# Kernel optimization log

Hardware: AMD Instinct MI355X
Metric: run time of the kernel (lower is better)

## Reference

```python
import jax, jax.numpy as jnp
import numpy as np

D_MODEL = 1024
NUM_HEADS = 16


def setup_inputs() -> dict:
    key = jax.random.key(0)
    ks = jax.random.split(key, 5)
    B, S, D = 2, 2048, D_MODEL
    x = jax.random.normal(ks[0], (B, S, D), dtype=jnp.float32)
    # nn.Linear(d_model, d_model, bias=False) weights, shape [out, in]
    scale = 1.0 / np.sqrt(D)
    Wq = jax.random.normal(ks[1], (D, D), dtype=jnp.float32) * scale
    Wk = jax.random.normal(ks[2], (D, D), dtype=jnp.float32) * scale
    Wv = jax.random.normal(ks[3], (D, D), dtype=jnp.float32) * scale
    Wo = jax.random.normal(ks[4], (D, D), dtype=jnp.float32) * scale
    return {"x": x, "Wq": Wq, "Wk": Wk, "Wv": Wv, "Wo": Wo}


def reference(x, Wq, Wk, Wv, Wo):
    B, S, D = x.shape
    H = NUM_HEADS
    dh = D // H
    # projections: x @ W.T (Linear without bias)
    q = (x @ Wq.T).reshape(B, S, H, dh).transpose(0, 2, 1, 3)  # [B,H,S,dh]
    k = (x @ Wk.T).reshape(B, S, H, dh).transpose(0, 2, 1, 3)
    v = (x @ Wv.T).reshape(B, S, H, dh).transpose(0, 2, 1, 3)
    scores = jnp.einsum("bhqd,bhkd->bhqk", q, k) / jnp.sqrt(jnp.float32(dh))
    # causal mask: positions j > i get -inf before softmax
    causal = jnp.triu(jnp.ones((S, S), dtype=bool), k=1)
    scores = jnp.where(causal, -jnp.inf, scores)
    attn = jax.nn.softmax(scores, axis=-1)  # [B,H,S,S]
    out = jnp.einsum("bhqk,bhkd->bhqd", attn, v)  # [B,H,S,dh]
    out = out.transpose(0, 2, 1, 3).reshape(B, S, D)
    return out @ Wo.T
```

## Files before the change

kernel.cpp:

```cpp
#include <hip/hip_runtime.h>

typedef __attribute__((ext_vector_type(8))) __bf16 bf16x8;
typedef __attribute__((ext_vector_type(4))) __bf16 bf16x4;
typedef __attribute__((ext_vector_type(2))) __bf16 bf16x2;
typedef __attribute__((ext_vector_type(4))) float f32x4;
typedef __attribute__((ext_vector_type(16))) float f32x16;
typedef __attribute__((ext_vector_type(4))) unsigned uint4v;

static constexpr int S = 2048;
static constexpr int D = 1024;
static constexpr int BATCH = 2;
static constexpr int M_ROWS = BATCH * S;

#define GLOAD_LDS16(gp, lp)                                                        \
  __builtin_amdgcn_global_load_lds((const __attribute__((address_space(1))) void*)(gp), \
                                   (__attribute__((address_space(3))) void*)(lp), 16, 0, 0)

__global__ __launch_bounds__(256) void cast_f32_bf16(const float* __restrict__ in,
                                                     __bf16* __restrict__ out) {
  int i = (blockIdx.x * 256 + threadIdx.x) * 4;
  *reinterpret_cast<bf16x4*>(out + i) =
      __builtin_convertvector(*reinterpret_cast<const f32x4*>(in + i), bf16x4);
}

__global__ __launch_bounds__(256) void cast_w4(const float* __restrict__ w0, const float* __restrict__ w1,
                                               const float* __restrict__ w2, const float* __restrict__ w3,
                                               __bf16* __restrict__ o0, __bf16* __restrict__ o1,
                                               __bf16* __restrict__ o2, __bf16* __restrict__ o3) {
  const float* in = blockIdx.y == 0 ? w0 : blockIdx.y == 1 ? w1 : blockIdx.y == 2 ? w2 : w3;
  __bf16* out = blockIdx.y == 0 ? o0 : blockIdx.y == 1 ? o1 : blockIdx.y == 2 ? o2 : o3;
  int i = (blockIdx.x * 256 + threadIdx.x) * 4;
  *reinterpret_cast<bf16x4*>(out + i) =
      __builtin_convertvector(*reinterpret_cast<const f32x4*>(in + i), bf16x4);
}

template <typename OutT>
__device__ __forceinline__ void gemm_core(const __bf16* __restrict__ A,
                                          const __bf16* __restrict__ Bm,
                                          OutT* __restrict__ C, int m0, int n0, int K, int ldc,
                                          __bf16* At, __bf16* Bt) {
  const int tid = threadIdx.x;
  const int w = tid >> 6, l = tid & 63;
  const int wr = w >> 1, wc = w & 1;
  const int ln = l & 15, gr = l >> 4;

  const int srow = w * 32 + (l >> 2);
  const int scol = (l & 3) * 8;
  const size_t aoff = (size_t)(m0 + srow) * K + scol;
  const size_t boff = (size_t)(n0 + srow) * K + scol;
  __bf16* lA = At + w * 2 * 512;
  __bf16* lB = Bt + w * 2 * 512;

  f32x4 acc[4][4] = {};

  for (int k0 = 0; k0 < K; k0 += 32) {
    __syncthreads();
    GLOAD_LDS16(A + aoff + k0, lA);
    GLOAD_LDS16(A + aoff + (size_t)16 * K + k0, lA + 512);
    GLOAD_LDS16(Bm + boff + k0, lB);
    GLOAD_LDS16(Bm + boff + (size_t)16 * K + k0, lB + 512);
    __syncthreads();

    bf16x8 af[4], bfr[4];
#pragma unroll
    for (int mi = 0; mi < 4; mi++)
      af[mi] = *reinterpret_cast<const bf16x8*>(&At[(wr * 64 + mi * 16 + ln) * 32 + gr * 8]);
#pragma unroll
    for (int ni = 0; ni < 4; ni++)
      bfr[ni] = *reinterpret_cast<const bf16x8*>(&Bt[(wc * 64 + ni * 16 + ln) * 32 + gr * 8]);
#pragma unroll
    for (int mi = 0; mi < 4; mi++)
#pragma unroll
      for (int ni = 0; ni < 4; ni++)
        acc[mi][ni] = __builtin_amdgcn_mfma_f32_16x16x32_bf16(af[mi], bfr[ni], acc[mi][ni], 0, 0, 0);
  }

#pragma unroll
  for (int mi = 0; mi < 4; mi++)
#pragma unroll
    for (int ni = 0; ni < 4; ni++)
#pragma unroll
      for (int r = 0; r < 4; r++) {
        int row = m0 + wr * 64 + mi * 16 + gr * 4 + r;
        int col = n0 + wc * 64 + ni * 16 + ln;
        float v = acc[mi][ni][r];
        if constexpr (__is_same(OutT, float))
          C[(size_t)row * ldc + col] = v;
        else
          C[(size_t)row * ldc + col] = (__bf16)v;
      }
}

__global__ __launch_bounds__(256) void qkv_gemm(const __bf16* __restrict__ xb,
                                                const __bf16* __restrict__ wq,
                                                const __bf16* __restrict__ wk,
                                                const __bf16* __restrict__ wv,
                                                __bf16* __restrict__ q, __bf16* __restrict__ k,
                                                __bf16* __restrict__ vt) {
  __shared__ __bf16 At[128 * 32];
  __shared__ __bf16 Bt[128 * 32];
  const int id = blockIdx.x;
  const __bf16 *A, *B;
  __bf16* C;
  int m0, n0, ldc;
  if (id < 512) {
    A = xb;
    B = (id < 256) ? wq : wk;
    C = (id < 256) ? q : k;
    int t = id & 255;
    m0 = (t >> 3) * 128;
    n0 = (t & 7) * 128;
    ldc = 1024;
  } else {
    int t = id - 512;
    A = wv;
    B = xb;
    C = vt;
    m0 = (t & 7) * 128;
    n0 = (t >> 3) * 128;
    ldc = 4096;
  }
  gemm_core<__bf16>(A, B, C, m0, n0, 1024, ldc, At, Bt);
}

__global__ __launch_bounds__(256) void wo_gemm(const __bf16* __restrict__ ob,
                                               const __bf16* __restrict__ wo,
                                               float* __restrict__ out) {
  __shared__ __bf16 At[128 * 32];
  __shared__ __bf16 Bt[128 * 32];
  gemm_core<float>(ob, wo, out, blockIdx.y * 128, blockIdx.x * 128, 1024, 1024, At, Bt);
}

__global__ __launch_bounds__(512, 2) void attn_kernel(const __bf16* __restrict__ Qb,
                                                      const __bf16* __restrict__ Kb,
                                                      const __bf16* __restrict__ VTb,
                                                      __bf16* __restrict__ Ob) {
  __shared__ __bf16 mo[8][64][32];
  __shared__ float mml[8][64][2];

  const int lin = blockIdx.x;
  const int wid = ((lin & 7) << 5) | (lin >> 3);
  const int bh = wid >> 3;
  const int ib = wid & 7;
  const int b = bh >> 4, h = bh & 15;

  const int tid = threadIdx.x;
  const int w = tid >> 6, l = tid & 63;
  const int q31 = l & 31, hi = l >> 5;
  const int pp = w & 3, hf = w >> 2;

  const int j = ib * 4 + pp;
  const int q0A = j * 32, q0B = (63 - j) * 32;
  const int nA = j + 1, nB = 64 - j;
  const int nhA = (nA + 1) >> 1, nhB = (nB + 1) >> 1;
  const int sA = hf ? nhA : 0, cA = hf ? nA - nhA : nhA;
  const int sB = hf ? nhB : 0, cB = hf ? nB - nhB : nhB;

  const __bf16* Qp = Qb + (size_t)b * S * D + h * 64;
  const __bf16* Kp = Kb + (size_t)b * S * D + h * 64;
  const __bf16* Vt = VTb + (size_t)(h * 64) * M_ROWS + b * S;

  const float SCALE2 = 0.125f * 1.44269504f;
  const float NEG = -1e30f;
  const float THR_RAW = 8.0f / SCALE2;

  bf16x8 qfA[4], qfB[4];
#pragma unroll
  for (int ds = 0; ds < 4; ds++) {
    qfA[ds] = *reinterpret_cast<const bf16x8*>(Qp + (size_t)(q0A + q31) * D + ds * 16 + hi * 8);
    qfB[ds] = *reinterpret_cast<const bf16x8*>(Qp + (size_t)(q0B + q31) * D + ds * 16 + hi * 8);
  }

  f32x16 oaccA[2] = {}, oaccB[2] = {};
  float mrA = NEG, lsA = 0.f, mrB = NEG, lsB = 0.f;

  auto loadK = [&](bf16x8 (&dst)[4], int kk) {
#pragma unroll
    for (int ds = 0; ds < 4; ds++)
      dst[ds] = *reinterpret_cast<const bf16x8*>(
          Kp + (size_t)(kk + q31) * D + ds * 16 + hi * 8);
  };
  auto loadV = [&](bf16x8 (&dst)[2][2], int kk) {
#pragma unroll
    for (int d0 = 0; d0 < 2; d0++)
#pragma unroll
      for (int ks = 0; ks < 2; ks++)
        dst[d0][ks] = *reinterpret_cast<const bf16x8*>(
            Vt + (size_t)(d0 * 32 + q31) * M_ROWS + kk + ks * 16 + hi * 8);
  };
  auto qk1 = [&](f32x16& st, bf16x8 (&kf)[4], bf16x8 (&qf)[4]) {
    f32x16 z = {};
#pragma unroll
    for (int ds = 0; ds < 4; ds++)
      z = __builtin_amdgcn_mfma_f32_32x32x16_bf16(kf[ds], qf[ds], z, 0, 0, 0);
    st = z;
  };
  auto pack2 = [](float x, float y) -> unsigned {
    bf16x2 p;
    p[0] = (__bf16)x;
    p[1] = (__bf16)y;
    return __builtin_bit_cast(unsigned, p);
  };
  auto maskmax = [&](f32x16& st, bool tail, float (&pv)[16]) -> float {
#pragma unroll
    for (int r = 0; r < 16; r++) {
      float v = st[r];
      if (tail) {
        int keyidx = (r & 3) + 8 * (r >> 2) + 4 * hi;
        v = (keyidx <= q31) ? v : NEG;
      }
      pv[r] = v;
    }
    float t8[8], t4[4];
#pragma unroll
    for (int ii = 0; ii < 8; ii++) t8[ii] = fmaxf(pv[ii], pv[ii + 8]);
#pragma unroll
    for (int ii = 0; ii < 4; ii++) t4[ii] = fmaxf(t8[ii], t8[ii + 4]);
    float tm = fmaxf(fmaxf(t4[0], t4[1]), fmaxf(t4[2], t4[3]));
    return fmaxf(tm, __shfl_xor(tm, 32));
  };
  auto rescale = [&](float& mr, float& ls, f32x16& o0, f32x16& o1, float tm) {
    float nm = fmaxf(mr, tm);
    float a = __builtin_exp2f((mr - nm) * SCALE2);
    mr = nm;
    ls *= a;
#pragma unroll
    for (int r = 0; r < 16; r++) o0[r] *= a;
#pragma unroll
    for (int r = 0; r < 16; r++) o1[r] *= a;
  };
  auto expsum = [&](float (&pv)[16], float mr, float& ls, unsigned (&dw)[8]) {
    const float mrs = mr * SCALE2;
#pragma unroll
    for (int r = 0; r < 16; r++)
      pv[r] = __builtin_exp2f(__builtin_fmaf(pv[r], SCALE2, -mrs));
    float s8[8], s4[4];
#pragma unroll
    for (int ii = 0; ii < 8; ii++) s8[ii] = pv[ii] + pv[ii + 8];
#pragma unroll
    for (int ii = 0; ii < 4; ii++) s4[ii] = s8[ii] + s8[ii + 4];
    float ps = (s4[0] + s4[1]) + (s4[2] + s4[3]);
    ps += __shfl_xor(ps, 32);
    ls += ps;
#pragma unroll
    for (int bb = 0; bb < 4; bb++) {
      dw[2 * bb] = pack2(pv[4 * bb], pv[4 * bb + 1]);
      dw[2 * bb + 1] = pack2(pv[4 * bb + 2], pv[4 * bb + 3]);
    }
  };
  auto pvmma = [&](unsigned (&dw)[8], bf16x8 (&vf)[2][2], f32x16& o0, f32x16& o1) {
#pragma unroll
    for (int ks = 0; ks < 2; ks++) {
      unsigned s0v = hi ? dw[4 * ks + 0] : dw[4 * ks + 2];
      unsigned s1v = hi ? dw[4 * ks + 1] : dw[4 * ks + 3];
      unsigned r0 = (unsigned)__shfl_xor((int)s0v, 32);
      unsigned r1 = (unsigned)__shfl_xor((int)s1v, 32);
      uint4v uv;
      uv.x = hi ? r0 : dw[4 * ks + 0];
      uv.y = hi ? r1 : dw[4 * ks + 1];
      uv.z = hi ? dw[4 * ks + 2] : r0;
      uv.w = hi ? dw[4 * ks + 3] : r1;
      bf16x8 pb = __builtin_bit_cast(bf16x8, uv);
      o0 = __builtin_amdgcn_mfma_f32_32x32x16_bf16(vf[0][ks], pb, o0, 0, 0, 0);
      o1 = __builtin_amdgcn_mfma_f32_32x32x16_bf16(vf[1][ks], pb, o1, 0, 0, 0);
    }
  };

  bf16x8 kfA[4], kfB[4], vfA[2][2], vfB[2][2];
  f32x16 stA, stB;

  if (cA > 0) {
    loadK(kfA, sA * 32);
    loadV(vfA, sA * 32);
  }
  loadK(kfB, sB * 32);
  loadV(vfB, sB * 32);

  for (int i2 = 0; i2 < cA; i2++) {
    __builtin_amdgcn_s_setprio(1);
    qk1(stA, kfA, qfA);
    qk1(stB, kfB, qfB);
    __builtin_amdgcn_s_setprio(0);
    if (i2 + 1 < cA) loadK(kfA, (sA + i2 + 1) * 32);
    if (i2 + 1 < cB) loadK(kfB, (sB + i2 + 1) * 32);

    float pvA[16], pvB[16];
    float tmA = maskmax(stA, sA + i2 == nA - 1, pvA);
    float tmB = maskmax(stB, sB + i2 == nB - 1, pvB);
    if (!__all((tmA - mrA <= THR_RAW) && (tmB - mrB <= THR_RAW))) {
      rescale(mrA, lsA, oaccA[0], oaccA[1], tmA);
      rescale(mrB, lsB, oaccB[0], oaccB[1], tmB);
    }
    unsigned dwA[8], dwB[8];
    expsum(pvA, mrA, lsA, dwA);
    expsum(pvB, mrB, lsB, dwB);
    __builtin_amdgcn_s_setprio(1);
    pvmma(dwA, vfA, oaccA[0], oaccA[1]);
    pvmma(dwB, vfB, oaccB[0], oaccB[1]);
    __builtin_amdgcn_s_setprio(0);
    if (i2 + 1 < cA) loadV(vfA, (sA + i2 + 1) * 32);
    if (i2 + 1 < cB) loadV(vfB, (sB + i2 + 1) * 32);
  }
  for (int i2 = cA; i2 < cB; i2++) {
    __builtin_amdgcn_s_setprio(1);
    qk1(stB, kfB, qfB);
    __builtin_amdgcn_s_setprio(0);
    if (i2 + 1 < cB) loadK(kfB, (sB + i2 + 1) * 32);
    float pvB[16];
    float tmB = maskmax(stB, sB + i2 == nB - 1, pvB);
    if (!__all(tmB - mrB <= THR_RAW)) rescale(mrB, lsB, oaccB[0], oaccB[1], tmB);
    unsigned dwB[8];
    expsum(pvB, mrB, lsB, dwB);
    __builtin_amdgcn_s_setprio(1);
    pvmma(dwB, vfB, oaccB[0], oaccB[1]);
    __builtin_amdgcn_s_setprio(0);
    if (i2 + 1 < cB) loadV(vfB, (sB + i2 + 1) * 32);
  }

  if (hf == 1) {
#pragma unroll
    for (int d0 = 0; d0 < 2; d0++) {
      bf16x8 pkA, pkB;
#pragma unroll
      for (int rr = 0; rr < 8; rr++) {
        pkA[rr] = (__bf16)oaccA[d0][rr];
        pkB[rr] = (__bf16)oaccB[d0][rr];
      }
      *reinterpret_cast<bf16x8*>(&mo[2 * pp + 0][l][d0 * 16]) = pkA;
      *reinterpret_cast<bf16x8*>(&mo[2 * pp + 1][l][d0 * 16]) = pkB;
      bf16x8 pkA2, pkB2;
#pragma unroll
      for (int rr = 0; rr < 8; rr++) {
        pkA2[rr] = (__bf16)oaccA[d0][8 + rr];
        pkB2[rr] = (__bf16)oaccB[d0][8 + rr];
      }
      *reinterpret_cast<bf16x8*>(&mo[2 * pp + 0][l][d0 * 16 + 8]) = pkA2;
      *reinterpret_cast<bf16x8*>(&mo[2 * pp + 1][l][d0 * 16 + 8]) = pkB2;
    }
    mml[2 * pp + 0][l][0] = mrA;
    mml[2 * pp + 0][l][1] = lsA;
    mml[2 * pp + 1][l][0] = mrB;
    mml[2 * pp + 1][l][1] = lsB;
  }
  __syncthreads();
  if (hf == 0) {
#pragma unroll
    for (int cc = 0; cc < 2; cc++) {
      const int slot = 2 * pp + cc;
      const int q0 = cc ? q0B : q0A;
      f32x16* oacc = cc ? oaccB : oaccA;
      float mr = cc ? mrB : mrA;
      float ls = cc ? lsB : lsA;
      float mr1 = mml[slot][l][0], ls1 = mml[slot][l][1];
      float mc = fmaxf(mr, mr1);
      float a0 = __builtin_exp2f((mr - mc) * SCALE2);
      float a1 = __builtin_exp2f((mr1 - mc) * SCALE2);
      float inv = 1.0f / (ls * a0 + ls1 * a1);
      float f0 = a0 * inv, f1 = a1 * inv;
      size_t row = (size_t)(b * S + q0 + q31);
#pragma unroll
      for (int d0 = 0; d0 < 2; d0++)
#pragma unroll
        for (int bb = 0; bb < 4; bb++) {
          bf16x4 ov;
#pragma unroll
          for (int rr = 0; rr < 4; rr++) {
            float part = (float)mo[slot][l][d0 * 16 + 4 * bb + rr];
            ov[rr] = (__bf16)(oacc[d0][4 * bb + rr] * f0 + part * f1);
          }
          *reinterpret_cast<bf16x4*>(Ob + row * D + h * 64 + d0 * 32 + 8 * bb + 4 * hi) = ov;
        }
    }
  }
}

extern "C" void kernel_launch(void* const* d_in, const int* in_sizes, int n_in,
                              void* d_out, int out_size, void* d_ws, size_t ws_size,
                              hipStream_t stream) {
  const float* x = (const float*)d_in[0];
  const float* Wq = (const float*)d_in[1];
  const float* Wk = (const float*)d_in[2];
  const float* Wv = (const float*)d_in[3];
  const float* Wo = (const float*)d_in[4];
  float* out = (float*)d_out;

  char* ws = (char*)d_ws;
  const size_t MB = 1024 * 1024;
  __bf16* xb = (__bf16*)(ws + 0 * MB);
  __bf16* qb = (__bf16*)(ws + 8 * MB);
  __bf16* kb = (__bf16*)(ws + 16 * MB);
  __bf16* vtb = (__bf16*)(ws + 24 * MB);
  __bf16* ob = (__bf16*)(ws + 32 * MB);
  __bf16* wqb = (__bf16*)(ws + 40 * MB);
  __bf16* wkb = (__bf16*)(ws + 42 * MB);
  __bf16* wvb = (__bf16*)(ws + 44 * MB);
  __bf16* wob = (__bf16*)(ws + 46 * MB);

  const int nx = M_ROWS * D;
  const int nw = D * D;

  cast_f32_bf16<<<nx / 4 / 256, 256, 0, stream>>>(x, xb);
  cast_w4<<<dim3(nw / 4 / 256, 4), 256, 0, stream>>>(Wq, Wk, Wv, Wo, wqb, wkb, wvb, wob);

  qkv_gemm<<<768, 256, 0, stream>>>(xb, wqb, wkb, wvb, qb, kb, vtb);

  attn_kernel<<<256, 512, 0, stream>>>(qb, kb, vtb, ob);

  wo_gemm<<<dim3(8, 32), 256, 0, stream>>>(ob, wob, out);
}
```

Baseline: 141.7 us.

## Split attention KV range across four wave groups with 4-way merge

The attention kernel now launches 1024-thread blocks and splits each query tile's causal KV range into four contiguous quarters instead of two halves. Each of the three non-leader wave groups writes its partial output, running max and sum to enlarged shared memory, and the leader merges four partial softmax states. The goal is more waves per block to hide latency and shorten the per-wave serial KV loop. In exchange it uses more LDS, drops the two-blocks-per-CU launch bound (which can raise register pressure or lower occupancy), and adds merge work.

```diff
diff --git a/kernel.cpp b/kernel.cpp
--- a/kernel.cpp
+++ b/kernel.cpp
@@ -131,12 +131,12 @@
   gemm_core<float>(ob, wo, out, blockIdx.y * 128, blockIdx.x * 128, 1024, 1024, At, Bt);
 }
 
-__global__ __launch_bounds__(512, 2) void attn_kernel(const __bf16* __restrict__ Qb,
-                                                      const __bf16* __restrict__ Kb,
-                                                      const __bf16* __restrict__ VTb,
-                                                      __bf16* __restrict__ Ob) {
-  __shared__ __bf16 mo[8][64][32];
-  __shared__ float mml[8][64][2];
+__global__ __launch_bounds__(1024) void attn_kernel(const __bf16* __restrict__ Qb,
+                                                    const __bf16* __restrict__ Kb,
+                                                    const __bf16* __restrict__ VTb,
+                                                    __bf16* __restrict__ Ob) {
+  __shared__ __bf16 mo[24][64][32];
+  __shared__ float mml[24][64][2];
 
   const int lin = blockIdx.x;
   const int wid = ((lin & 7) << 5) | (lin >> 3);
@@ -147,14 +147,13 @@
   const int tid = threadIdx.x;
   const int w = tid >> 6, l = tid & 63;
   const int q31 = l & 31, hi = l >> 5;
-  const int pp = w & 3, hf = w >> 2;
+  const int pp = w & 3, qq = w >> 2;
 
   const int j = ib * 4 + pp;
   const int q0A = j * 32, q0B = (63 - j) * 32;
   const int nA = j + 1, nB = 64 - j;
-  const int nhA = (nA + 1) >> 1, nhB = (nB + 1) >> 1;
-  const int sA = hf ? nhA : 0, cA = hf ? nA - nhA : nhA;
-  const int sB = hf ? nhB : 0, cB = hf ? nB - nhB : nhB;
+  const int sA = (nA * qq) >> 2, cA = ((nA * (qq + 1)) >> 2) - sA;
+  const int sB = (nB * qq) >> 2, cB = ((nB * (qq + 1)) >> 2) - sB;
 
   const __bf16* Qp = Qb + (size_t)b * S * D + h * 64;
   const __bf16* Kp = Kb + (size_t)b * S * D + h * 64;
@@ -273,8 +272,10 @@
     loadK(kfA, sA * 32);
     loadV(vfA, sA * 32);
   }
-  loadK(kfB, sB * 32);
-  loadV(vfB, sB * 32);
+  if (cB > 0) {
+    loadK(kfB, sB * 32);
+    loadV(vfB, sB * 32);
+  }
 
   for (int i2 = 0; i2 < cA; i2++) {
     __builtin_amdgcn_s_setprio(1);
@@ -317,46 +318,48 @@
     if (i2 + 1 < cB) loadV(vfB, (sB + i2 + 1) * 32);
   }
 
-  if (hf == 1) {
-#pragma unroll
-    for (int d0 = 0; d0 < 2; d0++) {
-      bf16x8 pkA, pkB;
-#pragma unroll
-      for (int rr = 0; rr < 8; rr++) {
-        pkA[rr] = (__bf16)oaccA[d0][rr];
-        pkB[rr] = (__bf16)oaccB[d0][rr];
+  if (qq != 0) {
+    const int base = (qq - 1) * 8 + pp * 2;
+#pragma unroll
+    for (int cc = 0; cc < 2; cc++) {
+      const f32x16* oacc = cc ? oaccB : oaccA;
+      const int slot = base + cc;
+#pragma unroll
+      for (int d0 = 0; d0 < 2; d0++) {
+        bf16x8 pk0, pk1;
+#pragma unroll
+        for (int rr = 0; rr < 8; rr++) {
+          pk0[rr] = (__bf16)oacc[d0][rr];
+          pk1[rr] = (__bf16)oacc[d0][8 + rr];
+        }
+        *reinterpret_cast<bf16x8*>(&mo[slot][l][d0 * 16]) = pk0;
+        *reinterpret_cast<bf16x8*>(&mo[slot][l][d0 * 16 + 8]) = pk1;
       }
-      *reinterpret_cast<bf16x8*>(&mo[2 * pp + 0][l][d0 * 16]) = pkA;
-      *reinterpret_cast<bf16x8*>(&mo[2 * pp + 1][l][d0 * 16]) = pkB;
-      bf16x8 pkA2, pkB2;
-#pragma unroll
-      for (int rr = 0; rr < 8; rr++) {
-        pkA2[rr] = (__bf16)oaccA[d0][8 + rr];
-        pkB2[rr] = (__bf16)oaccB[d0][8 + rr];
+      mml[slot][l][0] = cc ? mrB : mrA;
+      mml[slot][l][1] = cc ? lsB : lsA;
+    }
+  }
+  __syncthreads();
+  if (qq == 0) {
+#pragma unroll
+    for (int cc = 0; cc < 2; cc++) {
+      const int q0 = cc ? q0B : q0A;
+      const f32x16* oacc = cc ? oaccB : oaccA;
+      float m0v = cc ? mrB : mrA;
+      float l0v = cc ? lsB : lsA;
+      float mm[3], ll[3];
+#pragma unroll
+      for (int qx = 0; qx < 3; qx++) {
+        const int slot = qx * 8 + pp * 2 + cc;
+        mm[qx] = mml[slot][l][0];
+        ll[qx] = mml[slot][l][1];
       }
-      *reinterpret_cast<bf16x8*>(&mo[2 * pp + 0][l][d0 * 16 + 8]) = pkA2;
-      *reinterpret_cast<bf16x8*>(&mo[2 * pp + 1][l][d0 * 16 + 8]) = pkB2;
-    }
-    mml[2 * pp + 0][l][0] = mrA;
-    mml[2 * pp + 0][l][1] = lsA;
-    mml[2 * pp + 1][l][0] = mrB;
-    mml[2 * pp + 1][l][1] = lsB;
-  }
-  __syncthreads();
-  if (hf == 0) {
-#pragma unroll
-    for (int cc = 0; cc < 2; cc++) {
-      const int slot = 2 * pp + cc;
-      const int q0 = cc ? q0B : q0A;
-      f32x16* oacc = cc ? oaccB : oaccA;
-      float mr = cc ? mrB : mrA;
-      float ls = cc ? lsB : lsA;
-      float mr1 = mml[slot][l][0], ls1 = mml[slot][l][1];
-      float mc = fmaxf(mr, mr1);
-      float a0 = __builtin_exp2f((mr - mc) * SCALE2);
-      float a1 = __builtin_exp2f((mr1 - mc) * SCALE2);
-      float inv = 1.0f / (ls * a0 + ls1 * a1);
-      float f0 = a0 * inv, f1 = a1 * inv;
+      float mc = fmaxf(fmaxf(m0v, mm[0]), fmaxf(mm[1], mm[2]));
+      float f0 = __builtin_exp2f((m0v - mc) * SCALE2);
+      float f1 = __builtin_exp2f((mm[0] - mc) * SCALE2);
+      float f2 = __builtin_exp2f((mm[1] - mc) * SCALE2);
+      float f3 = __builtin_exp2f((mm[2] - mc) * SCALE2);
+      float inv = 1.0f / (l0v * f0 + ll[0] * f1 + ll[1] * f2 + ll[2] * f3);
       size_t row = (size_t)(b * S + q0 + q31);
 #pragma unroll
       for (int d0 = 0; d0 < 2; d0++)
@@ -365,8 +368,12 @@
           bf16x4 ov;
 #pragma unroll
           for (int rr = 0; rr < 4; rr++) {
-            float part = (float)mo[slot][l][d0 * 16 + 4 * bb + rr];
-            ov[rr] = (__bf16)(oacc[d0][4 * bb + rr] * f0 + part * f1);
+            const int idx = d0 * 16 + 4 * bb + rr;
+            float acc = oacc[d0][4 * bb + rr] * f0;
+            acc += (float)mo[0 * 8 + pp * 2 + cc][l][idx] * f1;
+            acc += (float)mo[1 * 8 + pp * 2 + cc][l][idx] * f2;
+            acc += (float)mo[2 * 8 + pp * 2 + cc][l][idx] * f3;
+            ov[rr] = (__bf16)(acc * inv);
           }
           *reinterpret_cast<bf16x4*>(Ob + row * D + h * 64 + d0 * 32 + 8 * bb + 4 * hi) = ov;
         }
@@ -404,7 +411,7 @@
 
   qkv_gemm<<<768, 256, 0, stream>>>(xb, wqb, wkb, wvb, qb, kb, vtb);
 
-  attn_kernel<<<256, 512, 0, stream>>>(qb, kb, vtb, ob);
+  attn_kernel<<<256, 1024, 0, stream>>>(qb, kb, vtb, ob);
 
   wo_gemm<<<dim3(8, 32), 256, 0, stream>>>(ob, wob, out);
 }
```

Result: slower. 403.6 us (+184.9%).
